# Optimization experiments

Hardware: AMD Instinct MI355X
Metric: run time of the kernel (lower is better)

## Reference

```python
import jax, jax.numpy as jnp
import numpy as np


def setup_inputs() -> dict:
    key = jax.random.key(0)
    ks = jax.random.split(key, 9)
    B, S, F = 16, 512, 1024
    scale = 1.0 / np.sqrt(2 * F)  # ~torch Linear init scale
    return {
        "v": jax.random.normal(ks[0], (B, S, F), jnp.float32),
        "t": jax.random.normal(ks[1], (B, S, F), jnp.float32),
        "a": jax.random.normal(ks[2], (B, S, F), jnp.float32),
        "W_tv": jax.random.normal(ks[3], (2 * F, F), jnp.float32) * scale,
        "b_tv": jnp.zeros((F,), jnp.float32),
        "W_ta": jax.random.normal(ks[4], (2 * F, F), jnp.float32) * scale,
        "b_ta": jnp.zeros((F,), jnp.float32),
        "W_av": jax.random.normal(ks[5], (2 * F, F), jnp.float32) * scale,
        "b_av": jnp.zeros((F,), jnp.float32),
    }


def _branch_feat(x1, x2, W, b):
    # tanh(Linear(cat(x1, x2)))  -- split weight to avoid materializing concat
    F = x1.shape[-1]
    W1, W2 = W[:F], W[F:]
    return jnp.tanh(jnp.einsum("bsf,fg->bsg", x1, W1)
                    + jnp.einsum("bsf,fg->bsg", x2, W2) + b)


def _attend_gate(q, feat):
    # softmax(q @ feat^T) @ q, gated by feat
    scores = jnp.einsum("bqf,bkf->bqk", q, feat)  # [B,S,S]
    p = jax.nn.softmax(scores, axis=-1)
    return jnp.einsum("bqk,bkf->bqf", p, q) * feat


def reference(v, t, a, W_tv, b_tv, W_ta, b_ta, W_av, b_av):
    Ftv = _branch_feat(t, v, W_tv, b_tv)
    Fta = _branch_feat(t, a, W_ta, b_ta)
    Fav = _branch_feat(a, v, W_av, b_av)
    Oatv = _attend_gate(a, Ftv)
    Ovta = _attend_gate(v, Fta)
    Otav = _attend_gate(t, Fav)
    return jnp.concatenate((Oatv, Ovta, Otav), axis=2)
```

## Files before the change

### kernel.cpp

```cpp
#include <hip/hip_runtime.h>

typedef unsigned short ushort_t;
typedef _Float16 f16x8 __attribute__((ext_vector_type(8)));
typedef float f32x4 __attribute__((ext_vector_type(4)));
typedef unsigned short u16x8 __attribute__((ext_vector_type(8)));

#define DEVINL __device__ __forceinline__

constexpr int B = 16, S = 512, F = 1024;
constexpr int M_ROWS = B * S;
constexpr size_t NX = (size_t)M_ROWS * F;
constexpr size_t NW = (size_t)F * (2 * F);

DEVINL ushort_t f2h(float f) { return __builtin_bit_cast(ushort_t, (_Float16)f); }
DEVINL float h2f(ushort_t h) { return (float)__builtin_bit_cast(_Float16, h); }

DEVINL void gload_lds16(const void* g, void* l) {
  __builtin_amdgcn_global_load_lds(
      (__attribute__((address_space(1))) void*)(g),
      (__attribute__((address_space(3))) void*)(l), 16, 0, 0);
}

DEVINL f32x4 mfma16h(f16x8 a, f16x8 b, f32x4 c) {
  return __builtin_amdgcn_mfma_f32_16x16x32_f16(a, b, c, 0, 0, 0);
}

template <int KSTEPS, int SPLIT_STEP>
DEVINL void gemm4p_core(const ushort_t* __restrict__ a1, const ushort_t* __restrict__ a2,
                        int lda, const ushort_t* __restrict__ bsrc, int ldb,
                        ushort_t* lds, int tid, f32x4 (&acc)[4][8]) {
  constexpr int BUF = 32768;
  constexpr int BOFF = 16384;
  constexpr int KM = KSTEPS - 1;
  const int lane = tid & 63, w = tid >> 6;
  const int wr = (w >> 1) * 64, wc = (w & 1) * 128;
  const int slog = (lane & 7) ^ ((lane >> 3) & 7);

  const int sl0 = ((lane >> 4) ^ (lane & 7)) * 8;
  const int sl1 = ((4 + (lane >> 4)) ^ (lane & 7)) * 8;
  const ushort_t* dsA0 = lds + (wr + (lane & 15)) * 64 + sl0;
  const ushort_t* dsA1 = lds + (wr + (lane & 15)) * 64 + sl1;
  const ushort_t* dsB0 = lds + BOFF + (wc + (lane & 15)) * 64 + sl0;
  const ushort_t* dsB1 = lds + BOFF + (wc + (lane & 15)) * 64 + sl1;

  const size_t ldaS = (size_t)lda, ldbS = (size_t)ldb;
  const ushort_t* gA1 = a1 + (size_t)(w * 16 + (lane >> 3)) * ldaS + slog * 8;
  const ushort_t* gA2 = a2 + (size_t)(w * 16 + (lane >> 3)) * ldaS + slog * 8;
  const ushort_t* gB  = bsrc + (size_t)(w * 16 + (lane >> 3)) * ldbS + slog * 8;
  ushort_t* dA = lds + (w * 16) * 64;
  ushort_t* dB = lds + BOFF + (w * 16) * 64;

  auto stA = [&](int bb, int ks, int h) {
    const ushort_t* base = ((SPLIT_STEP >= KSTEPS) || (ks < SPLIT_STEP)) ? gA1 : gA2;
    const ushort_t* s = base + (ks & (SPLIT_STEP - 1)) * 64 + (size_t)(h * 128) * ldaS;
    ushort_t* d = dA + bb * BUF + h * 8192;
    gload_lds16(s, d);
    gload_lds16(s + 8 * ldaS, d + 512);
  };
  auto stB = [&](int bb, int ks, int h) {
    const ushort_t* s = gB + ks * 64 + (size_t)(h * 128) * ldbS;
    ushort_t* d = dB + bb * BUF + h * 8192;
    gload_lds16(s, d);
    gload_lds16(s + 8 * ldbS, d + 512);
  };

#define BAR asm volatile("s_barrier" ::: "memory")
#define RDB(J)                                              \
  Bn0 = *(const f16x8*)(rB0 + (J) * 1024);                  \
  Bn1 = *(const f16x8*)(rB1 + (J) * 1024);                  \
  Bn2 = *(const f16x8*)(rB0 + ((J) + 1) * 1024);            \
  Bn3 = *(const f16x8*)(rB1 + ((J) + 1) * 1024);
#define PHASE_MM(JP)                                        \
  __builtin_amdgcn_s_setprio(1);                            \
  _Pragma("unroll")                                         \
  for (int i = 0; i < 4; ++i) {                             \
    acc[i][2 * (JP)]     = mfma16h(rA[i][0], Bc0, acc[i][2 * (JP)]);     \
    acc[i][2 * (JP)]     = mfma16h(rA[i][1], Bc1, acc[i][2 * (JP)]);     \
    acc[i][2 * (JP) + 1] = mfma16h(rA[i][0], Bc2, acc[i][2 * (JP) + 1]); \
    acc[i][2 * (JP) + 1] = mfma16h(rA[i][1], Bc3, acc[i][2 * (JP) + 1]); \
  }                                                         \
  __builtin_amdgcn_s_setprio(0);
#define SWAPB  Bc0 = Bn0; Bc1 = Bn1; Bc2 = Bn2; Bc3 = Bn3;
#define TILE(BB, T) {                                       \
  const int ksB = ((T) + 1) & KM;                           \
  const int ksA = ((T) + 2) & KM;                           \
  const ushort_t* rA0 = dsA0 + (BB) * BUF;                  \
  const ushort_t* rA1 = dsA1 + (BB) * BUF;                  \
  const ushort_t* rB0 = dsB0 + (BB) * BUF;                  \
  const ushort_t* rB1 = dsB1 + (BB) * BUF;                  \
  f16x8 rA[4][2];                                           \
  f16x8 Bc0, Bc1, Bc2, Bc3, Bn0, Bn1, Bn2, Bn3;             \
  _Pragma("unroll")                                         \
  for (int i = 0; i < 4; ++i) {                             \
    rA[i][0] = *(const f16x8*)(rA0 + i * 1024);             \
    rA[i][1] = *(const f16x8*)(rA1 + i * 1024);             \
  }                                                         \
  Bc0 = *(const f16x8*)(rB0);                               \
  Bc1 = *(const f16x8*)(rB1);                               \
  Bc2 = *(const f16x8*)(rB0 + 1024);                        \
  Bc3 = *(const f16x8*)(rB1 + 1024);                        \
  RDB(2)                                                    \
  stB(BB ^ 1, ksB, 0);                                      \
  BAR; PHASE_MM(0) BAR;                                     \
  SWAPB RDB(4)                                              \
  stB(BB ^ 1, ksB, 1);                                      \
  BAR; PHASE_MM(1) BAR;                                     \
  SWAPB RDB(6)                                              \
  stA(BB, ksA, 0);                                          \
  BAR; PHASE_MM(2) BAR;                                     \
  SWAPB                                                     \
  stA(BB, ksA, 1);                                          \
  BAR; PHASE_MM(3)                                          \
  asm volatile("s_waitcnt vmcnt(4)" ::: "memory");          \
  BAR;                                                      \
}

  stA(0, 0, 0); stA(0, 0, 1);
  stB(0, 0, 0); stB(0, 0, 1);
  stA(1, 1 & KM, 0); stA(1, 1 & KM, 1);
  asm volatile("s_waitcnt vmcnt(4)" ::: "memory");
  BAR;

  for (int t = 0; t < KSTEPS; t += 2) {
    TILE(0, t)
    TILE(1, t + 1)
  }
#undef TILE
#undef SWAPB
#undef PHASE_MM
#undef RDB
#undef BAR
}

__global__ __launch_bounds__(256) void split_x_kernel(
    const float* __restrict__ v, const float* __restrict__ t, const float* __restrict__ a,
    ushort_t* __restrict__ xh, ushort_t* __restrict__ xT) {
  __shared__ ushort_t tile[64][65];
  int mod = blockIdx.z;
  const float* src = (mod == 0) ? v : (mod == 1 ? t : a);
  int b = blockIdx.y;
  int s0 = (blockIdx.x >> 4) * 64;
  int f0 = (blockIdx.x & 15) * 64;
  int tid = threadIdx.x;
  ushort_t* xp = xh + mod * NX;
  ushort_t* xt = xT + mod * NX;
  int fl = (tid & 15) * 4;
#pragma unroll
  for (int r = 0; r < 4; ++r) {
    int sl = (tid >> 4) + r * 16;
    int row = b * S + s0 + sl;
    float4 x = *(const float4*)(src + (size_t)row * F + f0 + fl);
    ushort_t h0 = f2h(x.x), h1 = f2h(x.y), h2 = f2h(x.z), h3 = f2h(x.w);
    *(ushort4*)(xp + (size_t)row * F + f0 + fl) = make_ushort4(h0, h1, h2, h3);
    tile[sl][fl] = h0; tile[sl][fl + 1] = h1; tile[sl][fl + 2] = h2; tile[sl][fl + 3] = h3;
  }
  __syncthreads();
#pragma unroll
  for (int r = 0; r < 4; ++r) {
    int flr = (tid >> 4) + r * 16;
    int sl4 = (tid & 15) * 4;
    ushort4 o = make_ushort4(tile[sl4][flr], tile[sl4 + 1][flr],
                             tile[sl4 + 2][flr], tile[sl4 + 3][flr]);
    size_t tidx = ((size_t)(b * F + f0 + flr)) * S + s0 + sl4;
    *(ushort4*)(xt + tidx) = o;
  }
}

__global__ __launch_bounds__(256) void split_w_kernel(
    const float* __restrict__ w0, const float* __restrict__ w1, const float* __restrict__ w2,
    ushort_t* __restrict__ wtpack) {
  __shared__ ushort_t th[64][65];
  int br = blockIdx.z;
  const float* w = (br == 0) ? w0 : (br == 1 ? w1 : w2);
  int g0 = blockIdx.x * 64;
  int f0 = blockIdx.y * 64;
  int tid = threadIdx.x;
  int gl = (tid & 15) * 4;
#pragma unroll
  for (int r = 0; r < 4; ++r) {
    int fl = (tid >> 4) + r * 16;
    float4 x = *(const float4*)(w + (size_t)(f0 + fl) * F + g0 + gl);
    th[fl][gl] = f2h(x.x); th[fl][gl + 1] = f2h(x.y);
    th[fl][gl + 2] = f2h(x.z); th[fl][gl + 3] = f2h(x.w);
  }
  __syncthreads();
  ushort_t* op = wtpack + br * NW;
#pragma unroll
  for (int r = 0; r < 4; ++r) {
    int glr = (tid >> 4) + r * 16;
    int fl4 = (tid & 15) * 4;
    size_t o = (size_t)(g0 + glr) * (2 * F) + f0 + fl4;
    *(ushort4*)(op + o) = make_ushort4(th[fl4][glr], th[fl4 + 1][glr],
                                       th[fl4 + 2][glr], th[fl4 + 3][glr]);
  }
}

__global__ __launch_bounds__(512, 2) void feat_gemm_kernel(
    const ushort_t* __restrict__ xh, const ushort_t* __restrict__ wtpack,
    const float* __restrict__ b0, const float* __restrict__ b1, const float* __restrict__ b2,
    ushort_t* __restrict__ fpack) {
  constexpr int M1[3] = {1, 1, 2};
  constexpr int M2[3] = {0, 2, 0};
  __shared__ __attribute__((aligned(16))) ushort_t lds[2 * 32768];
  int br = blockIdx.z;
  int lin = blockIdx.x;
  int gm0 = ((lin & 7) * 4 + ((lin >> 3) & 3)) * 256;
  int gn0 = (lin >> 5) * 256;
  int tid = threadIdx.x, lane = tid & 63, w = tid >> 6;
  const ushort_t* a1 = xh + M1[br] * NX + (size_t)gm0 * F;
  const ushort_t* a2 = xh + M2[br] * NX + (size_t)gm0 * F;
  const ushort_t* bb = wtpack + br * NW + (size_t)gn0 * (2 * F);
  f32x4 acc[4][8] = {};
  gemm4p_core<32, 16>(a1, a2, F, bb, 2 * F, lds, tid, acc);
  const float* bias = (br == 0) ? b0 : (br == 1 ? b1 : b2);
  ushort_t* op = fpack + br * NX;
  int wr = (w >> 1) * 64, wc = (w & 1) * 128;
#pragma unroll
  for (int i = 0; i < 4; ++i)
#pragma unroll
    for (int j = 0; j < 8; ++j)
#pragma unroll
      for (int r = 0; r < 4; ++r) {
        int row = gm0 + wr + i * 16 + (lane >> 4) * 4 + r;
        int col = gn0 + wc + j * 16 + (lane & 15);
        op[(size_t)row * F + col] = f2h(tanhf(acc[i][j][r] + bias[col]));
      }
}

__global__ __launch_bounds__(512, 2) void attn_scores_kernel(
    const ushort_t* __restrict__ xh, const ushort_t* __restrict__ fpack,
    ushort_t* __restrict__ pbuf) {
  constexpr int QM[3] = {2, 0, 1};
  constexpr int BUFE = 20480;
  constexpr int BOFFE = 4096;
  __shared__ __attribute__((aligned(16))) ushort_t lds[3 * BUFE + 1024];
  float* redm = (float*)(lds + 3 * BUFE);
  int z = blockIdx.z;
  int br = z >> 4, b = z & 15;
  int gm0 = blockIdx.x * 128;
  int tid = threadIdx.x, lane = tid & 63, w = tid >> 6;
  int wm = w >> 2, wn = w & 3;
  int wr = wm * 64, wc = wn * 128;
  const ushort_t* qa = xh + QM[br] * NX + (size_t)(b * S + gm0) * F;
  const ushort_t* kb = fpack + br * NX + (size_t)(b * S) * F;

  const int scol = (((lane & 3) ^ ((lane >> 3) & 3)) * 8);
  const int foff = (lane & 15) * 32 + (((lane >> 4) ^ ((lane >> 1) & 3)) * 8);

  auto stA = [&](int sb, int ks) {
    const ushort_t* s = qa + (size_t)(w * 16 + (lane >> 2)) * F + ks * 32 + scol;
    gload_lds16(s, lds + sb * BUFE + w * 512);
  };
  auto stB = [&](int sb, int ks) {
#pragma unroll
    for (int g = 0; g < 4; ++g) {
      const ushort_t* s = kb + (size_t)(w * 64 + g * 16 + (lane >> 2)) * F + ks * 32 + scol;
      gload_lds16(s, lds + sb * BUFE + BOFFE + w * 2048 + g * 512);
    }
  };

  f32x4 acc[4][8] = {};
  stA(0, 0); stB(0, 0);
  stA(1, 1); stB(1, 1);
  asm volatile("s_waitcnt vmcnt(5)" ::: "memory");
  asm volatile("s_barrier" ::: "memory");

  for (int t = 0; t < 32; ++t) {
    const int cb = t % 3, sb = (t + 2) % 3;
    const int ks = (t + 2) & 31;
    stA(sb, ks); stB(sb, ks);
    const ushort_t* L = lds + cb * BUFE;
    f16x8 rA[4], rB[8];
#pragma unroll
    for (int i = 0; i < 4; ++i) rA[i] = *(const f16x8*)(L + (wr + i * 16) * 32 + foff);
#pragma unroll
    for (int j = 0; j < 8; ++j)
      rB[j] = *(const f16x8*)(L + BOFFE + (wc + j * 16) * 32 + foff);
    __builtin_amdgcn_s_setprio(1);
#pragma unroll
    for (int j = 0; j < 8; ++j)
#pragma unroll
      for (int i = 0; i < 4; ++i) acc[i][j] = mfma16h(rA[i], rB[j], acc[i][j]);
    __builtin_amdgcn_s_setprio(0);
    asm volatile("s_waitcnt vmcnt(5)" ::: "memory");
    asm volatile("s_barrier" ::: "memory");
  }

  float mx[4][4];
#pragma unroll
  for (int i = 0; i < 4; ++i)
#pragma unroll
    for (int r = 0; r < 4; ++r) {
      float m = acc[i][0][r];
#pragma unroll
      for (int j = 1; j < 8; ++j) m = fmaxf(m, acc[i][j][r]);
#pragma unroll
      for (int d = 1; d < 16; d <<= 1) m = fmaxf(m, __shfl_xor(m, d));
      mx[i][r] = m;
    }
  if ((lane & 15) == 0) {
#pragma unroll
    for (int i = 0; i < 4; ++i)
#pragma unroll
      for (int r = 0; r < 4; ++r)
        redm[wn * 128 + wr + i * 16 + (lane >> 4) * 4 + r] = mx[i][r];
  }
  __syncthreads();
  float inv[4][4];
#pragma unroll
  for (int i = 0; i < 4; ++i)
#pragma unroll
    for (int r = 0; r < 4; ++r) {
      int row = wr + i * 16 + (lane >> 4) * 4 + r;
      float fm = fmaxf(fmaxf(redm[row], redm[128 + row]),
                       fmaxf(redm[256 + row], redm[384 + row]));
      float s = 0.f;
#pragma unroll
      for (int j = 0; j < 8; ++j) {
        float e = expf(acc[i][j][r] - fm);
        acc[i][j][r] = e;
        s += e;
      }
#pragma unroll
      for (int d = 1; d < 16; d <<= 1) s += __shfl_xor(s, d);
      inv[i][r] = s;
    }
  __syncthreads();
  if ((lane & 15) == 0) {
#pragma unroll
    for (int i = 0; i < 4; ++i)
#pragma unroll
      for (int r = 0; r < 4; ++r)
        redm[wn * 128 + wr + i * 16 + (lane >> 4) * 4 + r] = inv[i][r];
  }
  __syncthreads();
  ushort_t* pout = pbuf + (size_t)z * S * S;
#pragma unroll
  for (int i = 0; i < 4; ++i)
#pragma unroll
    for (int r = 0; r < 4; ++r) {
      int row = wr + i * 16 + (lane >> 4) * 4 + r;
      float fs = (redm[row] + redm[128 + row]) + (redm[256 + row] + redm[384 + row]);
      float fi = 1.0f / fs;
#pragma unroll
      for (int j = 0; j < 8; ++j) {
        int col = wc + j * 16 + (lane & 15);
        pout[(size_t)(gm0 + row) * S + col] = f2h(acc[i][j][r] * fi);
      }
    }
}

__global__ __launch_bounds__(512, 2) void pv_gemm_kernel(
    const ushort_t* __restrict__ p, const ushort_t* __restrict__ xT,
    const ushort_t* __restrict__ fpack, float* __restrict__ out) {
  constexpr int QM[3] = {2, 0, 1};
  __shared__ __attribute__((aligned(16))) ushort_t lds[2 * 32768];
  int z = blockIdx.z;
  int br = z >> 4, b = z & 15;
  int gm0 = blockIdx.x * 256;
  int gn0 = blockIdx.y * 256;
  int tid = threadIdx.x, lane = tid & 63, w = tid >> 6;
  const ushort_t* pa = p + (size_t)z * S * S + (size_t)gm0 * S;
  const ushort_t* qt = xT + QM[br] * NX + (size_t)b * F * S + (size_t)gn0 * S;
  f32x4 acc[4][8] = {};
  gemm4p_core<8, 8>(pa, pa, S, qt, S, lds, tid, acc);
  const ushort_t* fp = fpack + br * NX;
  int wr = (w >> 1) * 64, wc = (w & 1) * 128;
#pragma unroll
  for (int i = 0; i < 4; ++i)
#pragma unroll
    for (int j = 0; j < 8; ++j)
#pragma unroll
      for (int r = 0; r < 4; ++r) {
        int row = gm0 + wr + i * 16 + (lane >> 4) * 4 + r;
        int col = gn0 + wc + j * 16 + (lane & 15);
        float fe = h2f(fp[(size_t)(b * S + row) * F + col]);
        out[(size_t)(b * S + row) * (3 * F) + br * F + col] = acc[i][j][r] * fe;
      }
}

extern "C" void kernel_launch(void* const* d_in, const int* in_sizes, int n_in,
                              void* d_out, int out_size, void* d_ws, size_t ws_size,
                              hipStream_t stream) {
  (void)in_sizes; (void)n_in; (void)out_size; (void)ws_size;
  const float* v = (const float*)d_in[0];
  const float* t = (const float*)d_in[1];
  const float* a = (const float*)d_in[2];
  const float* W_tv = (const float*)d_in[3];
  const float* b_tv = (const float*)d_in[4];
  const float* W_ta = (const float*)d_in[5];
  const float* b_ta = (const float*)d_in[6];
  const float* W_av = (const float*)d_in[7];
  const float* b_av = (const float*)d_in[8];
  float* out = (float*)d_out;

  ushort_t* xh = (ushort_t*)d_ws;
  ushort_t* xT = xh + 3 * NX;
  ushort_t* wtpack = xT + 3 * NX;
  ushort_t* fpack = wtpack + 3 * NW;
  ushort_t* pbuf = fpack + 3 * NX;

  split_x_kernel<<<dim3(128, 16, 3), 256, 0, stream>>>(v, t, a, xh, xT);
  split_w_kernel<<<dim3(16, 32, 3), 256, 0, stream>>>(W_tv, W_ta, W_av, wtpack);
  feat_gemm_kernel<<<dim3(128, 1, 3), 512, 0, stream>>>(xh, wtpack,
                                                        b_tv, b_ta, b_av, fpack);
  attn_scores_kernel<<<dim3(4, 1, 48), 512, 0, stream>>>(xh, fpack, pbuf);
  pv_gemm_kernel<<<dim3(2, 4, 48), 512, 0, stream>>>(pbuf, xT, fpack, out);
}
```

Baseline: 290.2 us.

## Fuse attention scores, softmax and PV GEMM into one kernel keeping P in LDS

Merges the scores+softmax kernel and the PV GEMM kernel into a single kernel. Each block handles 64 query rows across all 512 keys, keeps the normalized probabilities in swizzled LDS, then runs the PV product in two column passes. The fp16 P round trip through global memory and one launch go away. The grid is flattened to 384 blocks with XCD-aware index mapping, and staging drops from triple to double buffering with full vmcnt(0) waits. In exchange each block recomputes smaller tiles, pipelining is shallower, and the big LDS footprint (~138KB) may limit occupancy.

```diff
diff --git a/kernel.cpp b/kernel.cpp
--- a/kernel.cpp
+++ b/kernel.cpp
@@ -227,156 +227,171 @@
       }
 }
 
-__global__ __launch_bounds__(512, 2) void attn_scores_kernel(
-    const ushort_t* __restrict__ xh, const ushort_t* __restrict__ fpack,
-    ushort_t* __restrict__ pbuf) {
+__global__ __launch_bounds__(512, 2) void attn_fused_kernel(
+    const ushort_t* __restrict__ xh, const ushort_t* __restrict__ xT,
+    const ushort_t* __restrict__ fpack, float* __restrict__ out) {
   constexpr int QM[3] = {2, 0, 1};
-  constexpr int BUFE = 20480;
-  constexpr int BOFFE = 4096;
-  __shared__ __attribute__((aligned(16))) ushort_t lds[3 * BUFE + 1024];
-  float* redm = (float*)(lds + 3 * BUFE);
-  int z = blockIdx.z;
-  int br = z >> 4, b = z & 15;
-  int gm0 = blockIdx.x * 128;
+  constexpr int BUFQ = 18432;
+  constexpr int PVB = 16384;
+  constexpr int POFF = 36864;
+  constexpr int ROFF = 69632;
+  __shared__ __attribute__((aligned(16))) ushort_t lds[70656];
+  float* redm = (float*)(lds + ROFF);
+  int lin = blockIdx.x;
+  int xcd = lin & 7, g = lin >> 3;
+  int mblk = g & 7;
+  int zz = xcd * 6 + (g >> 3);
+  int br = zz >> 4, b = zz & 15;
+  int gm0 = mblk * 64;
   int tid = threadIdx.x, lane = tid & 63, w = tid >> 6;
-  int wm = w >> 2, wn = w & 3;
-  int wr = wm * 64, wc = wn * 128;
   const ushort_t* qa = xh + QM[br] * NX + (size_t)(b * S + gm0) * F;
   const ushort_t* kb = fpack + br * NX + (size_t)(b * S) * F;
-
   const int scol = (((lane & 3) ^ ((lane >> 3) & 3)) * 8);
   const int foff = (lane & 15) * 32 + (((lane >> 4) ^ ((lane >> 1) & 3)) * 8);
 
-  auto stA = [&](int sb, int ks) {
-    const ushort_t* s = qa + (size_t)(w * 16 + (lane >> 2)) * F + ks * 32 + scol;
-    gload_lds16(s, lds + sb * BUFE + w * 512);
+  auto stQA = [&](int sb, int ks) {
+    if (w < 4) {
+      const ushort_t* s = qa + (size_t)(w * 16 + (lane >> 2)) * F + ks * 32 + scol;
+      gload_lds16(s, lds + sb * BUFQ + w * 512);
+    }
   };
-  auto stB = [&](int sb, int ks) {
-#pragma unroll
-    for (int g = 0; g < 4; ++g) {
-      const ushort_t* s = kb + (size_t)(w * 64 + g * 16 + (lane >> 2)) * F + ks * 32 + scol;
-      gload_lds16(s, lds + sb * BUFE + BOFFE + w * 2048 + g * 512);
+  auto stQB = [&](int sb, int ks) {
+#pragma unroll
+    for (int gg = 0; gg < 4; ++gg) {
+      const ushort_t* s = kb + (size_t)(w * 64 + gg * 16 + (lane >> 2)) * F + ks * 32 + scol;
+      gload_lds16(s, lds + sb * BUFQ + 2048 + w * 2048 + gg * 512);
     }
   };
 
-  f32x4 acc[4][8] = {};
-  stA(0, 0); stB(0, 0);
-  stA(1, 1); stB(1, 1);
-  asm volatile("s_waitcnt vmcnt(5)" ::: "memory");
+  f32x4 acc[4][4] = {};
+  stQA(0, 0); stQB(0, 0);
+  asm volatile("s_waitcnt vmcnt(0)" ::: "memory");
   asm volatile("s_barrier" ::: "memory");
-
   for (int t = 0; t < 32; ++t) {
-    const int cb = t % 3, sb = (t + 2) % 3;
-    const int ks = (t + 2) & 31;
-    stA(sb, ks); stB(sb, ks);
-    const ushort_t* L = lds + cb * BUFE;
-    f16x8 rA[4], rB[8];
-#pragma unroll
-    for (int i = 0; i < 4; ++i) rA[i] = *(const f16x8*)(L + (wr + i * 16) * 32 + foff);
-#pragma unroll
-    for (int j = 0; j < 8; ++j)
-      rB[j] = *(const f16x8*)(L + BOFFE + (wc + j * 16) * 32 + foff);
+    int cur = t & 1;
+    int ks = (t + 1) & 31;
+    stQA(cur ^ 1, ks); stQB(cur ^ 1, ks);
+    const ushort_t* L = lds + cur * BUFQ;
+    f16x8 rA[4], rB[4];
+#pragma unroll
+    for (int i = 0; i < 4; ++i) rA[i] = *(const f16x8*)(L + (i * 16) * 32 + foff);
+#pragma unroll
+    for (int j = 0; j < 4; ++j)
+      rB[j] = *(const f16x8*)(L + 2048 + (w * 64 + j * 16) * 32 + foff);
     __builtin_amdgcn_s_setprio(1);
 #pragma unroll
-    for (int j = 0; j < 8; ++j)
+    for (int j = 0; j < 4; ++j)
 #pragma unroll
       for (int i = 0; i < 4; ++i) acc[i][j] = mfma16h(rA[i], rB[j], acc[i][j]);
     __builtin_amdgcn_s_setprio(0);
-    asm volatile("s_waitcnt vmcnt(5)" ::: "memory");
+    asm volatile("s_waitcnt vmcnt(0)" ::: "memory");
     asm volatile("s_barrier" ::: "memory");
   }
 
-  float mx[4][4];
 #pragma unroll
   for (int i = 0; i < 4; ++i)
 #pragma unroll
     for (int r = 0; r < 4; ++r) {
-      float m = acc[i][0][r];
-#pragma unroll
-      for (int j = 1; j < 8; ++j) m = fmaxf(m, acc[i][j][r]);
+      float m = fmaxf(fmaxf(acc[i][0][r], acc[i][1][r]),
+                      fmaxf(acc[i][2][r], acc[i][3][r]));
 #pragma unroll
       for (int d = 1; d < 16; d <<= 1) m = fmaxf(m, __shfl_xor(m, d));
-      mx[i][r] = m;
-    }
-  if ((lane & 15) == 0) {
+      if ((lane & 15) == 0) redm[w * 64 + i * 16 + (lane >> 4) * 4 + r] = m;
+    }
+  __syncthreads();
+  float sums[4][4];
+#pragma unroll
+  for (int i = 0; i < 4; ++i)
+#pragma unroll
+    for (int r = 0; r < 4; ++r) {
+      int row = i * 16 + (lane >> 4) * 4 + r;
+      float fm = redm[row];
+#pragma unroll
+      for (int ww = 1; ww < 8; ++ww) fm = fmaxf(fm, redm[ww * 64 + row]);
+      float s = 0.f;
+#pragma unroll
+      for (int j = 0; j < 4; ++j) {
+        float e = expf(acc[i][j][r] - fm);
+        acc[i][j][r] = e; s += e;
+      }
+#pragma unroll
+      for (int d = 1; d < 16; d <<= 1) s += __shfl_xor(s, d);
+      sums[i][r] = s;
+    }
+  __syncthreads();
+#pragma unroll
+  for (int i = 0; i < 4; ++i)
+#pragma unroll
+    for (int r = 0; r < 4; ++r)
+      if ((lane & 15) == 0) redm[w * 64 + i * 16 + (lane >> 4) * 4 + r] = sums[i][r];
+  __syncthreads();
+  ushort_t* P = lds + POFF;
+#pragma unroll
+  for (int i = 0; i < 4; ++i)
+#pragma unroll
+    for (int r = 0; r < 4; ++r) {
+      int row = i * 16 + (lane >> 4) * 4 + r;
+      float tot = 0.f;
+#pragma unroll
+      for (int ww = 0; ww < 8; ++ww) tot += redm[ww * 64 + row];
+      float inv = 1.0f / tot;
+#pragma unroll
+      for (int j = 0; j < 4; ++j) {
+        int col = w * 64 + j * 16 + (lane & 15);
+        P[row * 512 + (((col >> 3) ^ (row & 7)) * 8) + (col & 7)] =
+            f2h(acc[i][j][r] * inv);
+      }
+    }
+  __syncthreads();
+
+  const ushort_t* Bv = xT + QM[br] * NX + (size_t)b * F * S;
+  const ushort_t* fp = fpack + br * NX;
+  for (int pass = 0; pass < 2; ++pass) {
+    auto stPV = [&](int bb, int ks) {
+#pragma unroll
+      for (int gg = 0; gg < 4; ++gg) {
+        const ushort_t* s = Bv + (size_t)(pass * 512 + w * 64 + lane) * S + ks * 32 + gg * 8;
+        gload_lds16(s, lds + bb * PVB + gg * 4096 + w * 512);
+      }
+    };
+    f32x4 acc2[4][4] = {};
+    stPV(0, 0);
+    asm volatile("s_waitcnt vmcnt(0)" ::: "memory");
+    asm volatile("s_barrier" ::: "memory");
+    for (int t = 0; t < 16; ++t) {
+      int cur = t & 1;
+      stPV(cur ^ 1, (t + 1) & 15);
+      f16x8 pA[4], pB[4];
+      int aswz = ((t * 4 + (lane >> 4)) ^ (lane & 7)) * 8;
+#pragma unroll
+      for (int i = 0; i < 4; ++i)
+        pA[i] = *(const f16x8*)(P + (i * 16 + (lane & 15)) * 512 + aswz);
+#pragma unroll
+      for (int j = 0; j < 4; ++j)
+        pB[j] = *(const f16x8*)(lds + cur * PVB + (lane >> 4) * 4096 +
+                                (w * 64 + j * 16 + (lane & 15)) * 8);
+      __builtin_amdgcn_s_setprio(1);
+#pragma unroll
+      for (int j = 0; j < 4; ++j)
+#pragma unroll
+        for (int i = 0; i < 4; ++i) acc2[i][j] = mfma16h(pA[i], pB[j], acc2[i][j]);
+      __builtin_amdgcn_s_setprio(0);
+      asm volatile("s_waitcnt vmcnt(0)" ::: "memory");
+      asm volatile("s_barrier" ::: "memory");
+    }
 #pragma unroll
     for (int i = 0; i < 4; ++i)
 #pragma unroll
-      for (int r = 0; r < 4; ++r)
-        redm[wn * 128 + wr + i * 16 + (lane >> 4) * 4 + r] = mx[i][r];
-  }
-  __syncthreads();
-  float inv[4][4];
-#pragma unroll
-  for (int i = 0; i < 4; ++i)
-#pragma unroll
-    for (int r = 0; r < 4; ++r) {
-      int row = wr + i * 16 + (lane >> 4) * 4 + r;
-      float fm = fmaxf(fmaxf(redm[row], redm[128 + row]),
-                       fmaxf(redm[256 + row], redm[384 + row]));
-      float s = 0.f;
-#pragma unroll
-      for (int j = 0; j < 8; ++j) {
-        float e = expf(acc[i][j][r] - fm);
-        acc[i][j][r] = e;
-        s += e;
-      }
-#pragma unroll
-      for (int d = 1; d < 16; d <<= 1) s += __shfl_xor(s, d);
-      inv[i][r] = s;
-    }
-  __syncthreads();
-  if ((lane & 15) == 0) {
-#pragma unroll
-    for (int i = 0; i < 4; ++i)
-#pragma unroll
-      for (int r = 0; r < 4; ++r)
-        redm[wn * 128 + wr + i * 16 + (lane >> 4) * 4 + r] = inv[i][r];
-  }
-  __syncthreads();
-  ushort_t* pout = pbuf + (size_t)z * S * S;
-#pragma unroll
-  for (int i = 0; i < 4; ++i)
-#pragma unroll
-    for (int r = 0; r < 4; ++r) {
-      int row = wr + i * 16 + (lane >> 4) * 4 + r;
-      float fs = (redm[row] + redm[128 + row]) + (redm[256 + row] + redm[384 + row]);
-      float fi = 1.0f / fs;
-#pragma unroll
-      for (int j = 0; j < 8; ++j) {
-        int col = wc + j * 16 + (lane & 15);
-        pout[(size_t)(gm0 + row) * S + col] = f2h(acc[i][j][r] * fi);
-      }
-    }
-}
-
-__global__ __launch_bounds__(512, 2) void pv_gemm_kernel(
-    const ushort_t* __restrict__ p, const ushort_t* __restrict__ xT,
-    const ushort_t* __restrict__ fpack, float* __restrict__ out) {
-  constexpr int QM[3] = {2, 0, 1};
-  __shared__ __attribute__((aligned(16))) ushort_t lds[2 * 32768];
-  int z = blockIdx.z;
-  int br = z >> 4, b = z & 15;
-  int gm0 = blockIdx.x * 256;
-  int gn0 = blockIdx.y * 256;
-  int tid = threadIdx.x, lane = tid & 63, w = tid >> 6;
-  const ushort_t* pa = p + (size_t)z * S * S + (size_t)gm0 * S;
-  const ushort_t* qt = xT + QM[br] * NX + (size_t)b * F * S + (size_t)gn0 * S;
-  f32x4 acc[4][8] = {};
-  gemm4p_core<8, 8>(pa, pa, S, qt, S, lds, tid, acc);
-  const ushort_t* fp = fpack + br * NX;
-  int wr = (w >> 1) * 64, wc = (w & 1) * 128;
-#pragma unroll
-  for (int i = 0; i < 4; ++i)
-#pragma unroll
-    for (int j = 0; j < 8; ++j)
-#pragma unroll
-      for (int r = 0; r < 4; ++r) {
-        int row = gm0 + wr + i * 16 + (lane >> 4) * 4 + r;
-        int col = gn0 + wc + j * 16 + (lane & 15);
-        float fe = h2f(fp[(size_t)(b * S + row) * F + col]);
-        out[(size_t)(b * S + row) * (3 * F) + br * F + col] = acc[i][j][r] * fe;
-      }
+      for (int j = 0; j < 4; ++j)
+#pragma unroll
+        for (int r = 0; r < 4; ++r) {
+          int rowl = i * 16 + (lane >> 4) * 4 + r;
+          int col = pass * 512 + w * 64 + j * 16 + (lane & 15);
+          float fe = h2f(fp[(size_t)(b * S + gm0 + rowl) * F + col]);
+          out[(size_t)(b * S + gm0 + rowl) * (3 * F) + br * F + col] =
+              acc2[i][j][r] * fe;
+        }
+  }
 }
 
 extern "C" void kernel_launch(void* const* d_in, const int* in_sizes, int n_in,
@@ -398,12 +413,10 @@
   ushort_t* xT = xh + 3 * NX;
   ushort_t* wtpack = xT + 3 * NX;
   ushort_t* fpack = wtpack + 3 * NW;
-  ushort_t* pbuf = fpack + 3 * NX;
 
   split_x_kernel<<<dim3(128, 16, 3), 256, 0, stream>>>(v, t, a, xh, xT);
   split_w_kernel<<<dim3(16, 32, 3), 256, 0, stream>>>(W_tv, W_ta, W_av, wtpack);
   feat_gemm_kernel<<<dim3(128, 1, 3), 512, 0, stream>>>(xh, wtpack,
                                                         b_tv, b_ta, b_av, fpack);
-  attn_scores_kernel<<<dim3(4, 1, 48), 512, 0, stream>>>(xh, fpack, pbuf);
-  pv_gemm_kernel<<<dim3(2, 4, 48), 512, 0, stream>>>(pbuf, xT, fpack, out);
-}
+  attn_fused_kernel<<<dim3(384, 1, 1), 512, 0, stream>>>(xh, xT, fpack, out);
+}
```

Result: slower. 352.9 us (+21.6%).

## Halve GEMM tile width to 256x128 for feature and PV kernels

Applied to the files above, without the earlier changes.

Replaces the 256x256 GEMM core with a 256x128 variant for the feature GEMM and the PV GEMM, doubling the grid size of each (384->768 and 384->768 blocks). The K-step pipeline is rewritten into two MMA phases per tile with smaller B staging and reduced LDS. The aim is to fill the 256 CUs more evenly and lower register and LDS pressure. The cost is lower arithmetic intensity, with more A-tile reloads per output.

```diff
diff --git a/kernel.cpp b/kernel.cpp
--- a/kernel.cpp
+++ b/kernel.cpp
@@ -26,14 +26,14 @@
 }
 
 template <int KSTEPS, int SPLIT_STEP>
-DEVINL void gemm4p_core(const ushort_t* __restrict__ a1, const ushort_t* __restrict__ a2,
+DEVINL void gemm2p_core(const ushort_t* __restrict__ a1, const ushort_t* __restrict__ a2,
                         int lda, const ushort_t* __restrict__ bsrc, int ldb,
-                        ushort_t* lds, int tid, f32x4 (&acc)[4][8]) {
-  constexpr int BUF = 32768;
+                        ushort_t* lds, int tid, f32x4 (&acc)[4][4]) {
+  constexpr int BUF = 24576;
   constexpr int BOFF = 16384;
   constexpr int KM = KSTEPS - 1;
   const int lane = tid & 63, w = tid >> 6;
-  const int wr = (w >> 1) * 64, wc = (w & 1) * 128;
+  const int wr = (w >> 1) * 64, wc = (w & 1) * 64;
   const int slog = (lane & 7) ^ ((lane >> 3) & 7);
 
   const int sl0 = ((lane >> 4) ^ (lane & 7)) * 8;
@@ -46,9 +46,9 @@
   const size_t ldaS = (size_t)lda, ldbS = (size_t)ldb;
   const ushort_t* gA1 = a1 + (size_t)(w * 16 + (lane >> 3)) * ldaS + slog * 8;
   const ushort_t* gA2 = a2 + (size_t)(w * 16 + (lane >> 3)) * ldaS + slog * 8;
-  const ushort_t* gB  = bsrc + (size_t)(w * 16 + (lane >> 3)) * ldbS + slog * 8;
+  const ushort_t* gB  = bsrc + (size_t)(w * 8 + (lane >> 3)) * ldbS + slog * 8;
   ushort_t* dA = lds + (w * 16) * 64;
-  ushort_t* dB = lds + BOFF + (w * 16) * 64;
+  ushort_t* dB = lds + BOFF + (w * 8) * 64;
 
   auto stA = [&](int bb, int ks, int h) {
     const ushort_t* base = ((SPLIT_STEP >= KSTEPS) || (ks < SPLIT_STEP)) ? gA1 : gA2;
@@ -58,61 +58,49 @@
     gload_lds16(s + 8 * ldaS, d + 512);
   };
   auto stB = [&](int bb, int ks, int h) {
-    const ushort_t* s = gB + ks * 64 + (size_t)(h * 128) * ldbS;
-    ushort_t* d = dB + bb * BUF + h * 8192;
-    gload_lds16(s, d);
-    gload_lds16(s + 8 * ldbS, d + 512);
+    const ushort_t* s = gB + ks * 64 + (size_t)(h * 64) * ldbS;
+    gload_lds16(s, dB + bb * BUF + h * 4096);
   };
 
 #define BAR asm volatile("s_barrier" ::: "memory")
-#define RDB(J)                                              \
-  Bn0 = *(const f16x8*)(rB0 + (J) * 1024);                  \
-  Bn1 = *(const f16x8*)(rB1 + (J) * 1024);                  \
-  Bn2 = *(const f16x8*)(rB0 + ((J) + 1) * 1024);            \
-  Bn3 = *(const f16x8*)(rB1 + ((J) + 1) * 1024);
-#define PHASE_MM(JP)                                        \
-  __builtin_amdgcn_s_setprio(1);                            \
-  _Pragma("unroll")                                         \
-  for (int i = 0; i < 4; ++i) {                             \
-    acc[i][2 * (JP)]     = mfma16h(rA[i][0], Bc0, acc[i][2 * (JP)]);     \
-    acc[i][2 * (JP)]     = mfma16h(rA[i][1], Bc1, acc[i][2 * (JP)]);     \
-    acc[i][2 * (JP) + 1] = mfma16h(rA[i][0], Bc2, acc[i][2 * (JP) + 1]); \
-    acc[i][2 * (JP) + 1] = mfma16h(rA[i][1], Bc3, acc[i][2 * (JP) + 1]); \
-  }                                                         \
+#define MM2(J)                                                       \
+  __builtin_amdgcn_s_setprio(1);                                     \
+  _Pragma("unroll")                                                  \
+  for (int i = 0; i < 4; ++i) {                                      \
+    acc[i][(J)]     = mfma16h(rA[i][0], Bc0, acc[i][(J)]);           \
+    acc[i][(J)]     = mfma16h(rA[i][1], Bc1, acc[i][(J)]);           \
+    acc[i][(J) + 1] = mfma16h(rA[i][0], Bc2, acc[i][(J) + 1]);       \
+    acc[i][(J) + 1] = mfma16h(rA[i][1], Bc3, acc[i][(J) + 1]);       \
+  }                                                                  \
   __builtin_amdgcn_s_setprio(0);
-#define SWAPB  Bc0 = Bn0; Bc1 = Bn1; Bc2 = Bn2; Bc3 = Bn3;
-#define TILE(BB, T) {                                       \
-  const int ksB = ((T) + 1) & KM;                           \
-  const int ksA = ((T) + 2) & KM;                           \
-  const ushort_t* rA0 = dsA0 + (BB) * BUF;                  \
-  const ushort_t* rA1 = dsA1 + (BB) * BUF;                  \
-  const ushort_t* rB0 = dsB0 + (BB) * BUF;                  \
-  const ushort_t* rB1 = dsB1 + (BB) * BUF;                  \
-  f16x8 rA[4][2];                                           \
-  f16x8 Bc0, Bc1, Bc2, Bc3, Bn0, Bn1, Bn2, Bn3;             \
-  _Pragma("unroll")                                         \
-  for (int i = 0; i < 4; ++i) {                             \
-    rA[i][0] = *(const f16x8*)(rA0 + i * 1024);             \
-    rA[i][1] = *(const f16x8*)(rA1 + i * 1024);             \
-  }                                                         \
-  Bc0 = *(const f16x8*)(rB0);                               \
-  Bc1 = *(const f16x8*)(rB1);                               \
-  Bc2 = *(const f16x8*)(rB0 + 1024);                        \
-  Bc3 = *(const f16x8*)(rB1 + 1024);                        \
-  RDB(2)                                                    \
-  stB(BB ^ 1, ksB, 0);                                      \
-  BAR; PHASE_MM(0) BAR;                                     \
-  SWAPB RDB(4)                                              \
-  stB(BB ^ 1, ksB, 1);                                      \
-  BAR; PHASE_MM(1) BAR;                                     \
-  SWAPB RDB(6)                                              \
-  stA(BB, ksA, 0);                                          \
-  BAR; PHASE_MM(2) BAR;                                     \
-  SWAPB                                                     \
-  stA(BB, ksA, 1);                                          \
-  BAR; PHASE_MM(3)                                          \
-  asm volatile("s_waitcnt vmcnt(4)" ::: "memory");          \
-  BAR;                                                      \
+#define TILE2(BB, T) {                                               \
+  const int ksB = ((T) + 1) & KM;                                    \
+  const int ksA = ((T) + 2) & KM;                                    \
+  const ushort_t* rA0 = dsA0 + (BB) * BUF;                           \
+  const ushort_t* rA1 = dsA1 + (BB) * BUF;                           \
+  const ushort_t* rB0 = dsB0 + (BB) * BUF;                           \
+  const ushort_t* rB1 = dsB1 + (BB) * BUF;                           \
+  f16x8 rA[4][2];                                                    \
+  f16x8 Bc0, Bc1, Bc2, Bc3;                                          \
+  _Pragma("unroll")                                                  \
+  for (int i = 0; i < 4; ++i) {                                      \
+    rA[i][0] = *(const f16x8*)(rA0 + i * 1024);                      \
+    rA[i][1] = *(const f16x8*)(rA1 + i * 1024);                      \
+  }                                                                  \
+  Bc0 = *(const f16x8*)(rB0);                                        \
+  Bc1 = *(const f16x8*)(rB1);                                        \
+  Bc2 = *(const f16x8*)(rB0 + 1024);                                 \
+  Bc3 = *(const f16x8*)(rB1 + 1024);                                 \
+  stB(BB ^ 1, ksB, 0); stB(BB ^ 1, ksB, 1);                          \
+  BAR; MM2(0) BAR;                                                   \
+  Bc0 = *(const f16x8*)(rB0 + 2048);                                 \
+  Bc1 = *(const f16x8*)(rB1 + 2048);                                 \
+  Bc2 = *(const f16x8*)(rB0 + 3072);                                 \
+  Bc3 = *(const f16x8*)(rB1 + 3072);                                 \
+  stA(BB, ksA, 0); stA(BB, ksA, 1);                                  \
+  BAR; MM2(2)                                                        \
+  asm volatile("s_waitcnt vmcnt(4)" ::: "memory");                   \
+  BAR;                                                               \
 }
 
   stA(0, 0, 0); stA(0, 0, 1);
@@ -122,13 +110,11 @@
   BAR;
 
   for (int t = 0; t < KSTEPS; t += 2) {
-    TILE(0, t)
-    TILE(1, t + 1)
-  }
-#undef TILE
-#undef SWAPB
-#undef PHASE_MM
-#undef RDB
+    TILE2(0, t)
+    TILE2(1, t + 1)
+  }
+#undef TILE2
+#undef MM2
 #undef BAR
 }
 
@@ -201,24 +187,24 @@
     ushort_t* __restrict__ fpack) {
   constexpr int M1[3] = {1, 1, 2};
   constexpr int M2[3] = {0, 2, 0};
-  __shared__ __attribute__((aligned(16))) ushort_t lds[2 * 32768];
+  __shared__ __attribute__((aligned(16))) ushort_t lds[2 * 24576];
   int br = blockIdx.z;
   int lin = blockIdx.x;
   int gm0 = ((lin & 7) * 4 + ((lin >> 3) & 3)) * 256;
-  int gn0 = (lin >> 5) * 256;
+  int gn0 = (lin >> 5) * 128;
   int tid = threadIdx.x, lane = tid & 63, w = tid >> 6;
   const ushort_t* a1 = xh + M1[br] * NX + (size_t)gm0 * F;
   const ushort_t* a2 = xh + M2[br] * NX + (size_t)gm0 * F;
   const ushort_t* bb = wtpack + br * NW + (size_t)gn0 * (2 * F);
-  f32x4 acc[4][8] = {};
-  gemm4p_core<32, 16>(a1, a2, F, bb, 2 * F, lds, tid, acc);
+  f32x4 acc[4][4] = {};
+  gemm2p_core<32, 16>(a1, a2, F, bb, 2 * F, lds, tid, acc);
   const float* bias = (br == 0) ? b0 : (br == 1 ? b1 : b2);
   ushort_t* op = fpack + br * NX;
-  int wr = (w >> 1) * 64, wc = (w & 1) * 128;
-#pragma unroll
-  for (int i = 0; i < 4; ++i)
-#pragma unroll
-    for (int j = 0; j < 8; ++j)
+  int wr = (w >> 1) * 64, wc = (w & 1) * 64;
+#pragma unroll
+  for (int i = 0; i < 4; ++i)
+#pragma unroll
+    for (int j = 0; j < 4; ++j)
 #pragma unroll
       for (int r = 0; r < 4; ++r) {
         int row = gm0 + wr + i * 16 + (lane >> 4) * 4 + r;
@@ -354,22 +340,23 @@
     const ushort_t* __restrict__ p, const ushort_t* __restrict__ xT,
     const ushort_t* __restrict__ fpack, float* __restrict__ out) {
   constexpr int QM[3] = {2, 0, 1};
-  __shared__ __attribute__((aligned(16))) ushort_t lds[2 * 32768];
+  __shared__ __attribute__((aligned(16))) ushort_t lds[2 * 24576];
   int z = blockIdx.z;
   int br = z >> 4, b = z & 15;
-  int gm0 = blockIdx.x * 256;
-  int gn0 = blockIdx.y * 256;
+  int xblk = blockIdx.x;
+  int gm0 = (xblk & 1) * 256;
+  int gn0 = (xblk >> 1) * 128;
   int tid = threadIdx.x, lane = tid & 63, w = tid >> 6;
   const ushort_t* pa = p + (size_t)z * S * S + (size_t)gm0 * S;
   const ushort_t* qt = xT + QM[br] * NX + (size_t)b * F * S + (size_t)gn0 * S;
-  f32x4 acc[4][8] = {};
-  gemm4p_core<8, 8>(pa, pa, S, qt, S, lds, tid, acc);
+  f32x4 acc[4][4] = {};
+  gemm2p_core<8, 8>(pa, pa, S, qt, S, lds, tid, acc);
   const ushort_t* fp = fpack + br * NX;
-  int wr = (w >> 1) * 64, wc = (w & 1) * 128;
-#pragma unroll
-  for (int i = 0; i < 4; ++i)
-#pragma unroll
-    for (int j = 0; j < 8; ++j)
+  int wr = (w >> 1) * 64, wc = (w & 1) * 64;
+#pragma unroll
+  for (int i = 0; i < 4; ++i)
+#pragma unroll
+    for (int j = 0; j < 4; ++j)
 #pragma unroll
       for (int r = 0; r < 4; ++r) {
         int row = gm0 + wr + i * 16 + (lane >> 4) * 4 + r;
@@ -402,8 +389,8 @@
 
   split_x_kernel<<<dim3(128, 16, 3), 256, 0, stream>>>(v, t, a, xh, xT);
   split_w_kernel<<<dim3(16, 32, 3), 256, 0, stream>>>(W_tv, W_ta, W_av, wtpack);
-  feat_gemm_kernel<<<dim3(128, 1, 3), 512, 0, stream>>>(xh, wtpack,
+  feat_gemm_kernel<<<dim3(256, 1, 3), 512, 0, stream>>>(xh, wtpack,
                                                         b_tv, b_ta, b_av, fpack);
   attn_scores_kernel<<<dim3(4, 1, 48), 512, 0, stream>>>(xh, fpack, pbuf);
-  pv_gemm_kernel<<<dim3(2, 4, 48), 512, 0, stream>>>(pbuf, xT, fpack, out);
-}
+  pv_gemm_kernel<<<dim3(16, 1, 48), 512, 0, stream>>>(pbuf, xT, fpack, out);
+}
```

After: 270.9 us, median of 2. 1.07x faster.
